# Performance work log

Measured on AMD Instinct MI355X. Metric: run time of the kernel, lower is better.

The kernel has to match this reference:

```python
import jax, jax.numpy as jnp
import numpy as np

N, E, F_IN, H, G, OUT = 50000, 800000, 64, 128, 64, 16


def setup_inputs() -> dict:
    key = jax.random.key(0)
    ks = jax.random.split(key, 16)
    x = jax.random.normal(ks[0], (N, F_IN), dtype=jnp.float32)
    edge_index = jax.random.randint(ks[1], (2, E), 0, N, dtype=jnp.int64)
    edge_attr = jax.random.normal(ks[2], (E,), dtype=jnp.float32)
    batch = jnp.sort(jax.random.randint(ks[3], (N,), 0, G, dtype=jnp.int64))
    d_in = 2 * F_IN  # NaN mask doubles the feature dim
    s = lambda f: 1.0 / np.sqrt(f)
    W0 = jax.random.uniform(ks[4], (d_in, H), jnp.float32, -s(d_in), s(d_in))
    b0 = jnp.zeros((H,), jnp.float32)
    W1 = jax.random.uniform(ks[5], (H, H), jnp.float32, -s(H), s(H))
    b1 = jnp.zeros((H,), jnp.float32)
    W2 = jax.random.uniform(ks[6], (H, H), jnp.float32, -s(H), s(H))
    b2 = jnp.zeros((H,), jnp.float32)
    bn_gamma = 1.0 + 0.1 * jax.random.normal(ks[7], (H,), jnp.float32)
    bn_beta = 0.1 * jax.random.normal(ks[8], (H,), jnp.float32)
    bn_mean = 0.1 * jax.random.normal(ks[9], (H,), jnp.float32)
    bn_var = jnp.abs(1.0 + 0.1 * jax.random.normal(ks[10], (H,), jnp.float32))
    mW1 = jax.random.uniform(ks[11], (H, H), jnp.float32, -s(H), s(H))
    mb1 = jax.random.uniform(ks[12], (H,), jnp.float32, -s(H), s(H))
    mW2 = jax.random.uniform(ks[13], (H, OUT), jnp.float32, -s(H), s(H))
    mb2 = jax.random.uniform(ks[14], (OUT,), jnp.float32, -s(H), s(H))
    return dict(x=x, edge_index=edge_index, edge_attr=edge_attr, batch=batch,
                W0=W0, b0=b0, W1=W1, b1=b1, W2=W2, b2=b2,
                bn_gamma=bn_gamma, bn_beta=bn_beta, bn_mean=bn_mean, bn_var=bn_var,
                mW1=mW1, mb1=mb1, mW2=mW2, mb2=mb2)


def _gcn_conv(h_in, row, col, w, W, b, n):
    # PyG GCNConv with edge_weight, add_self_loops=True (self-loop weight 1)
    h = h_in @ W                                   # [N, H]
    deg = jax.ops.segment_sum(w, col, num_segments=n) + 1.0
    dinv = jnp.where(deg > 0, jax.lax.rsqrt(deg), 0.0)
    norm = dinv[row] * w * dinv[col]               # [E]
    agg = jax.ops.segment_sum(norm[:, None] * h[row], col, num_segments=n)
    agg = agg + (dinv * dinv)[:, None] * h         # self-loop contribution
    return agg + b


def _bn_eval(h, gamma, beta, mean, var, eps=1e-5):
    return (h - mean) * jax.lax.rsqrt(var + eps) * gamma + beta


def reference(x, edge_index, edge_attr, batch,
              W0, b0, W1, b1, W2, b2,
              bn_gamma, bn_beta, bn_mean, bn_var,
              mW1, mb1, mW2, mb2):
    n = x.shape[0]
    # handle_nan_features: zero NaNs and append binary NaN-mask channels
    nan_mask = jnp.isnan(x).astype(x.dtype)
    h = jnp.concatenate([jnp.nan_to_num(x, nan=0.0), nan_mask], axis=-1)
    w = jnp.abs(jnp.nan_to_num(edge_attr.reshape(-1), nan=0.0))
    row, col = edge_index[0], edge_index[1]
    for (W, b) in ((W0, b0), (W1, b1)):
        h = _gcn_conv(h, row, col, w, W, b, n)
        h = _bn_eval(h, bn_gamma, bn_beta, bn_mean, bn_var)
        h = jax.nn.relu(h)
        # dropout: identity in eval mode
    h = _gcn_conv(h, row, col, w, W2, b2, n)
    # global mean pool over graphs
    sums = jax.ops.segment_sum(h, batch, num_segments=G)
    cnts = jax.ops.segment_sum(jnp.ones((n,), h.dtype), batch, num_segments=G)
    g = sums / jnp.maximum(cnts, 1.0)[:, None]     # [G, H]
    g = jax.nn.gelu(g @ mW1 + mb1, approximate=False)
    return g @ mW2 + mb2                            # [G, OUT]
```

## Files before the change

kernel.cpp:

```cpp
#include <hip/hip_runtime.h>
#include <hip/hip_bf16.h>
#include <stdint.h>

#define HD 128
#define GD 64
#define OUTD 16

typedef unsigned short u16;
typedef __attribute__((ext_vector_type(8))) short short8;
typedef __attribute__((ext_vector_type(4))) float f32x4;

__device__ __forceinline__ float bf2f(u16 u) {
  union { uint32_t i; float f; } v; v.i = ((uint32_t)u) << 16; return v.f;
}
__device__ __forceinline__ u16 f2bf(float f) {
  union { __hip_bfloat16 h; u16 u; } v; v.h = __float2bfloat16(f); return v.u;
}

__global__ void zero_f_k(float* p, int n) {
  int i = blockIdx.x * 256 + threadIdx.x;
  if (i < n) p[i] = 0.f;
}
__global__ void zero_i_k(int* p, int n) {
  int i = blockIdx.x * 256 + threadIdx.x;
  if (i < n) p[i] = 0;
}

__global__ void detect_k(const int* ei, int* flag) {
  if (threadIdx.x == 0 && blockIdx.x == 0) {
    int all0 = 1;
    for (int k = 1; k < 128; k += 2) all0 &= (ei[k] == 0);
    *flag = all0;
  }
}

__global__ void convert_idx_k(const int* ei, const int* bt, int* idx, int* b32,
                              int E, int N, const int* flag) {
  int i = blockIdx.x * 256 + threadIdx.x;
  int is64 = *flag;
  if (i < 2 * E) {
    int v = is64 ? ei[2 * i] : ei[i];
    idx[i] = (v < 0) ? 0 : (v >= N ? N - 1 : v);
  }
  if (i < N) {
    int v = is64 ? bt[2 * i] : bt[i];
    b32[i] = (v < 0) ? 0 : (v >= GD ? GD - 1 : v);
  }
}

__global__ void count_k(const int* __restrict__ idx, int* __restrict__ cnt8,
                        int E, int N) {
  int e = blockIdx.x * 256 + threadIdx.x;
  if (e >= E) return;
  int k = blockIdx.x & 7;
  int col = idx[E + e];
  atomicAdd(&cnt8[k * N + col], 1);
}

__global__ void reduce_cnt_k(const int* __restrict__ cnt8, int* __restrict__ cnt, int N) {
  int n = blockIdx.x * 256 + threadIdx.x;
  if (n >= N) return;
  int s = 0;
#pragma unroll
  for (int k = 0; k < 8; ++k) s += cnt8[k * N + n];
  cnt[n] = s;
}

__global__ void scan1_k(const int* __restrict__ cnt, int* __restrict__ offs,
                        int* __restrict__ bsum, int Np) {
  __shared__ int s[1024];
  int i = blockIdx.x * 1024 + threadIdx.x;
  int v = (i < Np) ? cnt[i] : 0;
  s[threadIdx.x] = v;
  __syncthreads();
  for (int off = 1; off < 1024; off <<= 1) {
    int t = (threadIdx.x >= off) ? s[threadIdx.x - off] : 0;
    __syncthreads();
    s[threadIdx.x] += t;
    __syncthreads();
  }
  if (i < Np) offs[i] = s[threadIdx.x] - v;
  if (threadIdx.x == 1023) bsum[blockIdx.x] = s[1023];
}
__global__ void scan2_k(int* bsum, int nb) {
  if (threadIdx.x == 0 && blockIdx.x == 0) {
    int sum = 0;
    for (int i = 0; i < nb; ++i) { int v = bsum[i]; bsum[i] = sum; sum += v; }
  }
}
__global__ void scan3_k(int* __restrict__ offs, const int* __restrict__ bsum,
                        int Np, int E) {
  int i = blockIdx.x * 256 + threadIdx.x;
  if (i < Np) offs[i] = offs[i] + bsum[i >> 10];
  if (i == 0) offs[Np] = E;
}

__global__ void curs8_k(const int* __restrict__ offs, const int* __restrict__ cnt8,
                        int* __restrict__ curs8, int N) {
  int n = blockIdx.x * 256 + threadIdx.x;
  if (n >= N) return;
  int run = offs[n];
#pragma unroll
  for (int k = 0; k < 8; ++k) { curs8[k * N + n] = run; run += cnt8[k * N + n]; }
}

__global__ void fill_k(const int* __restrict__ idx, const float* __restrict__ ea,
                       int* __restrict__ curs8, int* __restrict__ srow,
                       float* __restrict__ sws, int E, int N) {
  int e = blockIdx.x * 256 + threadIdx.x;
  if (e >= E) return;
  int k = blockIdx.x & 7;
  int row = idx[e], col = idx[E + e];
  float a = ea[e];
  float w = isnan(a) ? 0.f : fabsf(a);
  int p = atomicAdd(&curs8[k * N + col], 1);
  srow[p] = row;
  sws[p] = w;
}

__global__ void deg_k(const int* __restrict__ offs, const float* __restrict__ sws,
                      float* __restrict__ dinv, int N) {
  int n = blockIdx.x * 256 + threadIdx.x;
  if (n >= N) return;
  int p = offs[n], pe = offs[n + 1];
  float s = 0.f;
  for (; p < pe; ++p) s += sws[p];
  dinv[n] = rsqrtf(s + 1.0f);
}

__global__ void normcsc_k(const int* __restrict__ offs, const int* __restrict__ srow,
                          const float* __restrict__ sws, const float* __restrict__ dinv,
                          float* __restrict__ snorm, int N) {
  int n = blockIdx.x * 256 + threadIdx.x;
  if (n >= N) return;
  float dc = dinv[n];
  int p = offs[n], pe = offs[n + 1];
  for (; p < pe; ++p) snorm[p] = dinv[srow[p]] * sws[p] * dc;
}

__global__ void build_h0_k(const float* __restrict__ x, u16* __restrict__ A, int N) {
  int i = blockIdx.x * 256 + threadIdx.x;
  if (i >= N * HD) return;
  int n = i >> 7, f = i & 127;
  float v;
  if (f < 64) { float u = x[n * 64 + f];      v = isnan(u) ? 0.f : u; }
  else        { float u = x[n * 64 + f - 64]; v = isnan(u) ? 1.f : 0.f; }
  A[i] = f2bf(v);
}

__global__ void convw_k(const float* __restrict__ W, u16* __restrict__ Wt) {
  int i = blockIdx.x * 256 + threadIdx.x;
  if (i >= HD * HD) return;
  int n = i >> 7, k = i & 127;
  Wt[i] = f2bf(W[k * HD + n]);
}

__global__ __launch_bounds__(256)
void gemm_k(const u16* __restrict__ A, const u16* __restrict__ Wt,
            u16* __restrict__ B, int N) {
  __shared__ u16 sw[128 * 136];
  const int t = threadIdx.x;
  {
    const uint32_t* src = (const uint32_t*)Wt;
    uint32_t* dst = (uint32_t*)sw;
#pragma unroll
    for (int k = 0; k < 32; ++k) {
      int q = t + k * 256;
      int r = q >> 6;
      int u = q & 63;
      dst[r * 68 + u] = src[r * 64 + u];
    }
  }
  __syncthreads();
  const int w = t >> 6;
  const int lane = t & 63;
  const int m = lane & 15;
  const int qd = lane >> 4;
  const int arow = blockIdx.x * 64 + w * 16 + m;
  short8 afr[4];
  if (arow < N) {
    const short8* ap = (const short8*)(A + (size_t)arow * HD);
#pragma unroll
    for (int s = 0; s < 4; ++s) afr[s] = ap[4 * s + qd];
  } else {
    short8 z = {0, 0, 0, 0, 0, 0, 0, 0};
#pragma unroll
    for (int s = 0; s < 4; ++s) afr[s] = z;
  }
  const int orow = blockIdx.x * 64 + w * 16 + qd * 4;
#pragma unroll
  for (int c = 0; c < 8; ++c) {
    f32x4 acc = {0.f, 0.f, 0.f, 0.f};
    const int n = c * 16 + m;
#pragma unroll
    for (int s = 0; s < 4; ++s) {
      short8 bfr = *(const short8*)(sw + n * 136 + 32 * s + 8 * qd);
      acc = __builtin_amdgcn_mfma_f32_16x16x32_bf16(afr[s], bfr, acc, 0, 0, 0);
    }
#pragma unroll
    for (int r = 0; r < 4; ++r) {
      int rr = orow + r;
      if (rr < N) B[(size_t)rr * HD + n] = f2bf(acc[r]);
    }
  }
}

__global__ __launch_bounds__(256)
void aggregate_k(const int* __restrict__ offs, const int* __restrict__ srow,
                 const float* __restrict__ snorm, const u16* __restrict__ B,
                 const float* __restrict__ dinv, const float* __restrict__ bias,
                 const float* __restrict__ gamma, const float* __restrict__ beta,
                 const float* __restrict__ mean, const float* __restrict__ var,
                 int do_bn, u16* __restrict__ A, int N) {
  int tid = blockIdx.x * 256 + threadIdx.x;
  int n = tid >> 5;
  if (n >= N) return;
  int f4 = (tid & 31) << 2;
  float d = dinv[n];
  ushort4 bu = *(const ushort4*)(B + (size_t)n * HD + f4);
  float ax = d * d * bf2f(bu.x) + bias[f4 + 0];
  float ay = d * d * bf2f(bu.y) + bias[f4 + 1];
  float az = d * d * bf2f(bu.z) + bias[f4 + 2];
  float aw = d * d * bf2f(bu.w) + bias[f4 + 3];

  int p = offs[n], pe = offs[n + 1];
  for (; p + 1 < pe; p += 2) {
    int r0 = srow[p], r1 = srow[p + 1];
    float w0 = snorm[p], w1 = snorm[p + 1];
    ushort4 h0 = *(const ushort4*)(B + (size_t)r0 * HD + f4);
    ushort4 h1 = *(const ushort4*)(B + (size_t)r1 * HD + f4);
    ax += w0 * bf2f(h0.x) + w1 * bf2f(h1.x);
    ay += w0 * bf2f(h0.y) + w1 * bf2f(h1.y);
    az += w0 * bf2f(h0.z) + w1 * bf2f(h1.z);
    aw += w0 * bf2f(h0.w) + w1 * bf2f(h1.w);
  }
  if (p < pe) {
    int r0 = srow[p];
    float w0 = snorm[p];
    ushort4 h0 = *(const ushort4*)(B + (size_t)r0 * HD + f4);
    ax += w0 * bf2f(h0.x); ay += w0 * bf2f(h0.y);
    az += w0 * bf2f(h0.z); aw += w0 * bf2f(h0.w);
  }
  if (do_bn) {
    float s0 = gamma[f4 + 0] * rsqrtf(var[f4 + 0] + 1e-5f);
    float s1 = gamma[f4 + 1] * rsqrtf(var[f4 + 1] + 1e-5f);
    float s2 = gamma[f4 + 2] * rsqrtf(var[f4 + 2] + 1e-5f);
    float s3 = gamma[f4 + 3] * rsqrtf(var[f4 + 3] + 1e-5f);
    ax = (ax - mean[f4 + 0]) * s0 + beta[f4 + 0];
    ay = (ay - mean[f4 + 1]) * s1 + beta[f4 + 1];
    az = (az - mean[f4 + 2]) * s2 + beta[f4 + 2];
    aw = (aw - mean[f4 + 3]) * s3 + beta[f4 + 3];
    ax = ax > 0.f ? ax : 0.f;
    ay = ay > 0.f ? ay : 0.f;
    az = az > 0.f ? az : 0.f;
    aw = aw > 0.f ? aw : 0.f;
  }
  ushort4 o;
  o.x = f2bf(ax); o.y = f2bf(ay); o.z = f2bf(az); o.w = f2bf(aw);
  *(ushort4*)(A + (size_t)n * HD + f4) = o;
}

__global__ void start_k(const int* __restrict__ b32, int* __restrict__ start, int N) {
  int b = threadIdx.x;
  if (b > GD) return;
  int lo = 0, hi = N;
  while (lo < hi) {
    int mid = (lo + hi) >> 1;
    if (b32[mid] < b) lo = mid + 1; else hi = mid;
  }
  start[b] = lo;
}

__global__ __launch_bounds__(128)
void pool1_k(const u16* __restrict__ A, const int* __restrict__ start,
             float* __restrict__ sums) {
  int b = blockIdx.y;
  int s = start[b], e = start[b + 1];
  int len = e - s;
  if (len <= 0) return;
  int nch = gridDim.x;
  int ch = (len + nch - 1) / nch;
  int lo = s + blockIdx.x * ch;
  int hi = lo + ch; if (hi > e) hi = e;
  if (lo >= hi) return;
  int j = threadIdx.x;
  float a0 = 0.f, a1 = 0.f, a2 = 0.f, a3 = 0.f;
  int n = lo;
  for (; n + 3 < hi; n += 4) {
    a0 += bf2f(A[(size_t)(n + 0) * HD + j]);
    a1 += bf2f(A[(size_t)(n + 1) * HD + j]);
    a2 += bf2f(A[(size_t)(n + 2) * HD + j]);
    a3 += bf2f(A[(size_t)(n + 3) * HD + j]);
  }
  for (; n < hi; ++n) a0 += bf2f(A[(size_t)n * HD + j]);
  unsafeAtomicAdd(&sums[b * HD + j], (a0 + a1) + (a2 + a3));
}

__global__ __launch_bounds__(128)
void mlp_k(const float* __restrict__ sums, const int* __restrict__ start,
           const float* __restrict__ mW1, const float* __restrict__ mb1,
           const float* __restrict__ mW2, const float* __restrict__ mb2,
           float* __restrict__ out) {
  __shared__ float sg[128];
  __shared__ float st[128];
  int b = blockIdx.x, j = threadIdx.x;
  int cnt = start[b + 1] - start[b];
  float inv = 1.0f / (float)(cnt > 0 ? cnt : 1);
  sg[j] = sums[b * HD + j] * inv;
  __syncthreads();
  float s = mb1[j];
#pragma unroll 4
  for (int i = 0; i < 128; ++i) s += sg[i] * mW1[i * 128 + j];
  float ge = 0.5f * s * (1.0f + erff(s * 0.70710678118654752f));
  st[j] = ge;
  __syncthreads();
  if (j < OUTD) {
    float o = mb2[j];
#pragma unroll 4
    for (int k = 0; k < 128; ++k) o += st[k] * mW2[k * OUTD + j];
    out[b * OUTD + j] = o;
  }
}

extern "C" void kernel_launch(void* const* d_in, const int* in_sizes, int n_in,
                              void* d_out, int out_size, void* d_ws, size_t ws_size,
                              hipStream_t stream) {
  const float* x   = (const float*)d_in[0];
  const int* ei    = (const int*)d_in[1];
  const float* ea  = (const float*)d_in[2];
  const int* bt    = (const int*)d_in[3];
  const float* W0  = (const float*)d_in[4];
  const float* b0  = (const float*)d_in[5];
  const float* W1  = (const float*)d_in[6];
  const float* b1  = (const float*)d_in[7];
  const float* W2  = (const float*)d_in[8];
  const float* b2  = (const float*)d_in[9];
  const float* bng = (const float*)d_in[10];
  const float* bnb = (const float*)d_in[11];
  const float* bnm = (const float*)d_in[12];
  const float* bnv = (const float*)d_in[13];
  const float* mW1 = (const float*)d_in[14];
  const float* mb1 = (const float*)d_in[15];
  const float* mW2 = (const float*)d_in[16];
  const float* mb2 = (const float*)d_in[17];
  float* out = (float*)d_out;

  const int N = in_sizes[0] / 64;
  const int E = in_sizes[2];

  char* ws = (char*)d_ws;
  size_t NB2 = (size_t)N * HD * 2;
  u16* A       = (u16*)(ws);
  u16* B       = (u16*)(ws + NB2);
  char* q      = ws + 2 * NB2;
  u16* Wt0     = (u16*)q;              q += (size_t)HD * HD * 2;
  u16* Wt1     = (u16*)q;              q += (size_t)HD * HD * 2;
  u16* Wt2     = (u16*)q;              q += (size_t)HD * HD * 2;
  float* snorm = (float*)q;            q += (size_t)E * 4;
  int*   srow  = (int*)q;              q += (size_t)E * 4;
  float* sws   = (float*)q;            q += (size_t)E * 4;
  int*   idx   = (int*)q;              q += (size_t)2 * E * 4;
  float* dinv  = (float*)q;            q += (size_t)N * 4;
  int*   cnt8  = (int*)q;              q += (size_t)8 * N * 4;
  int*   curs8 = (int*)q;              q += (size_t)8 * N * 4;
  int*   cnt   = (int*)q;              q += (size_t)N * 4;
  int*   offs  = (int*)q;              q += (size_t)(N + 2) * 4;
  int*   b32   = (int*)q;              q += (size_t)N * 4;
  int*   bsum  = (int*)q;              q += 64 * 4;
  float* sums  = (float*)q;            q += GD * HD * 4;
  int*   strt  = (int*)q;              q += 68 * 4;
  int*   flag  = (int*)q;

  const int NH = N * HD;
  dim3 blk(256);
  int gNH = (NH + 255) / 256;
  int gE  = (E + 255) / 256;
  int gN  = (N + 255) / 256;
  int gCv = (2 * E + 255) / 256;
  int gW  = (HD * HD + 255) / 256;
  int nb1024 = (N + 1023) / 1024;

  detect_k<<<1, 64, 0, stream>>>(ei, flag);
  convert_idx_k<<<gCv, blk, 0, stream>>>(ei, bt, idx, b32, E, N, flag);
  zero_i_k<<<(8 * N + 255) / 256, blk, 0, stream>>>(cnt8, 8 * N);
  zero_f_k<<<(GD * HD + 255) / 256, blk, 0, stream>>>(sums, GD * HD);
  convw_k<<<gW, blk, 0, stream>>>(W0, Wt0);
  convw_k<<<gW, blk, 0, stream>>>(W1, Wt1);
  convw_k<<<gW, blk, 0, stream>>>(W2, Wt2);
  count_k<<<gE, blk, 0, stream>>>(idx, cnt8, E, N);
  reduce_cnt_k<<<gN, blk, 0, stream>>>(cnt8, cnt, N);
  scan1_k<<<nb1024, 1024, 0, stream>>>(cnt, offs, bsum, N);
  scan2_k<<<1, 64, 0, stream>>>(bsum, nb1024);
  scan3_k<<<gN, blk, 0, stream>>>(offs, bsum, N, E);
  curs8_k<<<gN, blk, 0, stream>>>(offs, cnt8, curs8, N);
  fill_k<<<gE, blk, 0, stream>>>(idx, ea, curs8, srow, sws, E, N);
  deg_k<<<gN, blk, 0, stream>>>(offs, sws, dinv, N);
  normcsc_k<<<gN, blk, 0, stream>>>(offs, srow, sws, dinv, snorm, N);
  build_h0_k<<<gNH, blk, 0, stream>>>(x, A, N);

  int gGemm = (N + 63) / 64;
  int gAgg  = (N * 32 + 255) / 256;

  gemm_k<<<gGemm, 256, 0, stream>>>(A, Wt0, B, N);
  aggregate_k<<<gAgg, blk, 0, stream>>>(offs, srow, snorm, B, dinv, b0,
                                        bng, bnb, bnm, bnv, 1, A, N);
  gemm_k<<<gGemm, 256, 0, stream>>>(A, Wt1, B, N);
  aggregate_k<<<gAgg, blk, 0, stream>>>(offs, srow, snorm, B, dinv, b1,
                                        bng, bnb, bnm, bnv, 1, A, N);
  gemm_k<<<gGemm, 256, 0, stream>>>(A, Wt2, B, N);
  aggregate_k<<<gAgg, blk, 0, stream>>>(offs, srow, snorm, B, dinv, b2,
                                        bng, bnb, bnm, bnv, 0, A, N);

  start_k<<<1, 128, 0, stream>>>(b32, strt, N);
  dim3 pgrid(16, GD);
  pool1_k<<<pgrid, 128, 0, stream>>>(A, strt, sums);
  mlp_k<<<GD, 128, 0, stream>>>(sums, strt, mW1, mb1, mW2, mb2, out);
}
```

Measured before the change: 407.1 us.

## Pack CSC row index and edge weight into interleaved int2 arrays

Replaces the separate srow/sws/snorm arrays with one interleaved int2 CSC array holding source index and weight, normalized in place. Edge indices are likewise packed as int2 (row, col) pairs. The atomic-counter replication factor rises from 8 to 16 to spread contention in count and fill. The aim is to cut separate memory streams and halve the number of loads per edge in aggregation and preprocessing, in exchange for larger replicated count and cursor arrays.

```diff
diff --git a/kernel.cpp b/kernel.cpp
--- a/kernel.cpp
+++ b/kernel.cpp
@@ -5,6 +5,7 @@
 #define HD 128
 #define GD 64
 #define OUTD 16
+#define NR 16
 
 typedef unsigned short u16;
 typedef __attribute__((ext_vector_type(8))) short short8;
@@ -34,13 +35,16 @@
   }
 }
 
-__global__ void convert_idx_k(const int* ei, const int* bt, int* idx, int* b32,
+__global__ void convert_idx_k(const int* ei, const int* bt, int2* eidx, int* b32,
                               int E, int N, const int* flag) {
   int i = blockIdx.x * 256 + threadIdx.x;
   int is64 = *flag;
-  if (i < 2 * E) {
-    int v = is64 ? ei[2 * i] : ei[i];
-    idx[i] = (v < 0) ? 0 : (v >= N ? N - 1 : v);
+  if (i < E) {
+    int r = is64 ? ei[2 * i] : ei[i];
+    int c = is64 ? ei[2 * (E + i)] : ei[E + i];
+    r = (r < 0) ? 0 : (r >= N ? N - 1 : r);
+    c = (c < 0) ? 0 : (c >= N ? N - 1 : c);
+    eidx[i] = make_int2(r, c);
   }
   if (i < N) {
     int v = is64 ? bt[2 * i] : bt[i];
@@ -48,21 +52,20 @@
   }
 }
 
-__global__ void count_k(const int* __restrict__ idx, int* __restrict__ cnt8,
+__global__ void count_k(const int2* __restrict__ eidx, int* __restrict__ cntR,
                         int E, int N) {
   int e = blockIdx.x * 256 + threadIdx.x;
   if (e >= E) return;
-  int k = blockIdx.x & 7;
-  int col = idx[E + e];
-  atomicAdd(&cnt8[k * N + col], 1);
-}
-
-__global__ void reduce_cnt_k(const int* __restrict__ cnt8, int* __restrict__ cnt, int N) {
+  int k = blockIdx.x & (NR - 1);
+  atomicAdd(&cntR[k * N + eidx[e].y], 1);
+}
+
+__global__ void reduce_cnt_k(const int* __restrict__ cntR, int* __restrict__ cnt, int N) {
   int n = blockIdx.x * 256 + threadIdx.x;
   if (n >= N) return;
   int s = 0;
 #pragma unroll
-  for (int k = 0; k < 8; ++k) s += cnt8[k * N + n];
+  for (int k = 0; k < NR; ++k) s += cntR[k * N + n];
   cnt[n] = s;
 }
 
@@ -95,47 +98,48 @@
   if (i == 0) offs[Np] = E;
 }
 
-__global__ void curs8_k(const int* __restrict__ offs, const int* __restrict__ cnt8,
-                        int* __restrict__ curs8, int N) {
+__global__ void cursR_k(const int* __restrict__ offs, const int* __restrict__ cntR,
+                        int* __restrict__ cursR, int N) {
   int n = blockIdx.x * 256 + threadIdx.x;
   if (n >= N) return;
   int run = offs[n];
 #pragma unroll
-  for (int k = 0; k < 8; ++k) { curs8[k * N + n] = run; run += cnt8[k * N + n]; }
-}
-
-__global__ void fill_k(const int* __restrict__ idx, const float* __restrict__ ea,
-                       int* __restrict__ curs8, int* __restrict__ srow,
-                       float* __restrict__ sws, int E, int N) {
+  for (int k = 0; k < NR; ++k) { cursR[k * N + n] = run; run += cntR[k * N + n]; }
+}
+
+__global__ void fill_k(const int2* __restrict__ eidx, const float* __restrict__ ea,
+                       int* __restrict__ cursR, int2* __restrict__ csc, int E, int N) {
   int e = blockIdx.x * 256 + threadIdx.x;
   if (e >= E) return;
-  int k = blockIdx.x & 7;
-  int row = idx[e], col = idx[E + e];
+  int k = blockIdx.x & (NR - 1);
+  int2 rc = eidx[e];
   float a = ea[e];
   float w = isnan(a) ? 0.f : fabsf(a);
-  int p = atomicAdd(&curs8[k * N + col], 1);
-  srow[p] = row;
-  sws[p] = w;
-}
-
-__global__ void deg_k(const int* __restrict__ offs, const float* __restrict__ sws,
+  int p = atomicAdd(&cursR[k * N + rc.y], 1);
+  csc[p] = make_int2(rc.x, __float_as_int(w));
+}
+
+__global__ void deg_k(const int* __restrict__ offs, const int2* __restrict__ csc,
                       float* __restrict__ dinv, int N) {
   int n = blockIdx.x * 256 + threadIdx.x;
   if (n >= N) return;
   int p = offs[n], pe = offs[n + 1];
   float s = 0.f;
-  for (; p < pe; ++p) s += sws[p];
+  for (; p < pe; ++p) s += __int_as_float(csc[p].y);
   dinv[n] = rsqrtf(s + 1.0f);
 }
 
-__global__ void normcsc_k(const int* __restrict__ offs, const int* __restrict__ srow,
-                          const float* __restrict__ sws, const float* __restrict__ dinv,
-                          float* __restrict__ snorm, int N) {
+__global__ void normcsc_k(const int* __restrict__ offs, int2* __restrict__ csc,
+                          const float* __restrict__ dinv, int N) {
   int n = blockIdx.x * 256 + threadIdx.x;
   if (n >= N) return;
   float dc = dinv[n];
   int p = offs[n], pe = offs[n + 1];
-  for (; p < pe; ++p) snorm[p] = dinv[srow[p]] * sws[p] * dc;
+  for (; p < pe; ++p) {
+    int2 v = csc[p];
+    v.y = __float_as_int(dinv[v.x] * __int_as_float(v.y) * dc);
+    csc[p] = v;
+  }
 }
 
 __global__ void build_h0_k(const float* __restrict__ x, u16* __restrict__ A, int N) {
@@ -206,12 +210,12 @@
 }
 
 __global__ __launch_bounds__(256)
-void aggregate_k(const int* __restrict__ offs, const int* __restrict__ srow,
-                 const float* __restrict__ snorm, const u16* __restrict__ B,
-                 const float* __restrict__ dinv, const float* __restrict__ bias,
-                 const float* __restrict__ gamma, const float* __restrict__ beta,
-                 const float* __restrict__ mean, const float* __restrict__ var,
-                 int do_bn, u16* __restrict__ A, int N) {
+void aggregate_k(const int* __restrict__ offs, const int2* __restrict__ csc,
+                 const u16* __restrict__ B, const float* __restrict__ dinv,
+                 const float* __restrict__ bias, const float* __restrict__ gamma,
+                 const float* __restrict__ beta, const float* __restrict__ mean,
+                 const float* __restrict__ var, int do_bn,
+                 u16* __restrict__ A, int N) {
   int tid = blockIdx.x * 256 + threadIdx.x;
   int n = tid >> 5;
   if (n >= N) return;
@@ -225,19 +229,19 @@
 
   int p = offs[n], pe = offs[n + 1];
   for (; p + 1 < pe; p += 2) {
-    int r0 = srow[p], r1 = srow[p + 1];
-    float w0 = snorm[p], w1 = snorm[p + 1];
-    ushort4 h0 = *(const ushort4*)(B + (size_t)r0 * HD + f4);
-    ushort4 h1 = *(const ushort4*)(B + (size_t)r1 * HD + f4);
+    int2 e0 = csc[p], e1 = csc[p + 1];
+    float w0 = __int_as_float(e0.y), w1 = __int_as_float(e1.y);
+    ushort4 h0 = *(const ushort4*)(B + (size_t)e0.x * HD + f4);
+    ushort4 h1 = *(const ushort4*)(B + (size_t)e1.x * HD + f4);
     ax += w0 * bf2f(h0.x) + w1 * bf2f(h1.x);
     ay += w0 * bf2f(h0.y) + w1 * bf2f(h1.y);
     az += w0 * bf2f(h0.z) + w1 * bf2f(h1.z);
     aw += w0 * bf2f(h0.w) + w1 * bf2f(h1.w);
   }
   if (p < pe) {
-    int r0 = srow[p];
-    float w0 = snorm[p];
-    ushort4 h0 = *(const ushort4*)(B + (size_t)r0 * HD + f4);
+    int2 e0 = csc[p];
+    float w0 = __int_as_float(e0.y);
+    ushort4 h0 = *(const ushort4*)(B + (size_t)e0.x * HD + f4);
     ax += w0 * bf2f(h0.x); ay += w0 * bf2f(h0.y);
     az += w0 * bf2f(h0.z); aw += w0 * bf2f(h0.w);
   }
@@ -356,13 +360,11 @@
   u16* Wt0     = (u16*)q;              q += (size_t)HD * HD * 2;
   u16* Wt1     = (u16*)q;              q += (size_t)HD * HD * 2;
   u16* Wt2     = (u16*)q;              q += (size_t)HD * HD * 2;
-  float* snorm = (float*)q;            q += (size_t)E * 4;
-  int*   srow  = (int*)q;              q += (size_t)E * 4;
-  float* sws   = (float*)q;            q += (size_t)E * 4;
-  int*   idx   = (int*)q;              q += (size_t)2 * E * 4;
+  int2* csc    = (int2*)q;             q += (size_t)E * 8;
+  int2* eidx   = (int2*)q;             q += (size_t)E * 8;
   float* dinv  = (float*)q;            q += (size_t)N * 4;
-  int*   cnt8  = (int*)q;              q += (size_t)8 * N * 4;
-  int*   curs8 = (int*)q;              q += (size_t)8 * N * 4;
+  int*   cntR  = (int*)q;              q += (size_t)NR * N * 4;
+  int*   cursR = (int*)q;              q += (size_t)NR * N * 4;
   int*   cnt   = (int*)q;              q += (size_t)N * 4;
   int*   offs  = (int*)q;              q += (size_t)(N + 2) * 4;
   int*   b32   = (int*)q;              q += (size_t)N * 4;
@@ -376,39 +378,38 @@
   int gNH = (NH + 255) / 256;
   int gE  = (E + 255) / 256;
   int gN  = (N + 255) / 256;
-  int gCv = (2 * E + 255) / 256;
   int gW  = (HD * HD + 255) / 256;
   int nb1024 = (N + 1023) / 1024;
 
   detect_k<<<1, 64, 0, stream>>>(ei, flag);
-  convert_idx_k<<<gCv, blk, 0, stream>>>(ei, bt, idx, b32, E, N, flag);
-  zero_i_k<<<(8 * N + 255) / 256, blk, 0, stream>>>(cnt8, 8 * N);
+  convert_idx_k<<<gE, blk, 0, stream>>>(ei, bt, eidx, b32, E, N, flag);
+  zero_i_k<<<(NR * N + 255) / 256, blk, 0, stream>>>(cntR, NR * N);
   zero_f_k<<<(GD * HD + 255) / 256, blk, 0, stream>>>(sums, GD * HD);
   convw_k<<<gW, blk, 0, stream>>>(W0, Wt0);
   convw_k<<<gW, blk, 0, stream>>>(W1, Wt1);
   convw_k<<<gW, blk, 0, stream>>>(W2, Wt2);
-  count_k<<<gE, blk, 0, stream>>>(idx, cnt8, E, N);
-  reduce_cnt_k<<<gN, blk, 0, stream>>>(cnt8, cnt, N);
+  count_k<<<gE, blk, 0, stream>>>(eidx, cntR, E, N);
+  reduce_cnt_k<<<gN, blk, 0, stream>>>(cntR, cnt, N);
   scan1_k<<<nb1024, 1024, 0, stream>>>(cnt, offs, bsum, N);
   scan2_k<<<1, 64, 0, stream>>>(bsum, nb1024);
   scan3_k<<<gN, blk, 0, stream>>>(offs, bsum, N, E);
-  curs8_k<<<gN, blk, 0, stream>>>(offs, cnt8, curs8, N);
-  fill_k<<<gE, blk, 0, stream>>>(idx, ea, curs8, srow, sws, E, N);
-  deg_k<<<gN, blk, 0, stream>>>(offs, sws, dinv, N);
-  normcsc_k<<<gN, blk, 0, stream>>>(offs, srow, sws, dinv, snorm, N);
+  cursR_k<<<gN, blk, 0, stream>>>(offs, cntR, cursR, N);
+  fill_k<<<gE, blk, 0, stream>>>(eidx, ea, cursR, csc, E, N);
+  deg_k<<<gN, blk, 0, stream>>>(offs, csc, dinv, N);
+  normcsc_k<<<gN, blk, 0, stream>>>(offs, csc, dinv, N);
   build_h0_k<<<gNH, blk, 0, stream>>>(x, A, N);
 
   int gGemm = (N + 63) / 64;
   int gAgg  = (N * 32 + 255) / 256;
 
   gemm_k<<<gGemm, 256, 0, stream>>>(A, Wt0, B, N);
-  aggregate_k<<<gAgg, blk, 0, stream>>>(offs, srow, snorm, B, dinv, b0,
+  aggregate_k<<<gAgg, blk, 0, stream>>>(offs, csc, B, dinv, b0,
                                         bng, bnb, bnm, bnv, 1, A, N);
   gemm_k<<<gGemm, 256, 0, stream>>>(A, Wt1, B, N);
-  aggregate_k<<<gAgg, blk, 0, stream>>>(offs, srow, snorm, B, dinv, b1,
+  aggregate_k<<<gAgg, blk, 0, stream>>>(offs, csc, B, dinv, b1,
                                         bng, bnb, bnm, bnv, 1, A, N);
   gemm_k<<<gGemm, 256, 0, stream>>>(A, Wt2, B, N);
-  aggregate_k<<<gAgg, blk, 0, stream>>>(offs, srow, snorm, B, dinv, b2,
+  aggregate_k<<<gAgg, blk, 0, stream>>>(offs, csc, B, dinv, b2,
                                         bng, bnb, bnm, bnv, 0, A, N);
 
   start_k<<<1, 128, 0, stream>>>(b32, strt, N);
```

Result: slower. 419.4 us (+3.0%).
